# Performance work log

Hardware: AMD Instinct MI355X
Metric: run time of the kernel (lower is better)

Reference implementation:

```python
import jax, jax.numpy as jnp
import numpy as np

B, K, D, H, A = 8192, 10, 64, 128, 16
E = K * (K - 1)
# lexicographic ordered pairs (i,j), i != j -- matches adj.nonzero() and sorted(Dict.keys())
_PAIRS = np.array([(i, j) for i in range(K) for j in range(K) if i != j], dtype=np.int32)
SRC = jnp.asarray(_PAIRS[:, 0])  # message for edge (i,j) is aggregated at node i (row)
DST = jnp.asarray(_PAIRS[:, 1])


def setup_inputs() -> dict:
    key = jax.random.key(0)
    k1, k2, k3, k4, k5, k6 = jax.random.split(key, 6)
    F = D + H + A  # node MLP input dim
    return {
        "states": jax.random.normal(k1, (B, K, D), jnp.float32),
        "action_vec": jax.random.normal(k2, (B, K, A), jnp.float32),
        # one Linear(2D -> H) per ordered pair, stacked [E, 2D, H]
        "W_edge": jax.random.normal(k3, (E, 2 * D, H), jnp.float32) * (1.0 / np.sqrt(2 * D)),
        "b_edge": jax.random.normal(k4, (E, H), jnp.float32) * 0.01,
        # one Linear(D+H+A -> D) per node, stacked [K, F, D]
        "W_node": jax.random.normal(k5, (K, F, D), jnp.float32) * (1.0 / np.sqrt(F)),
        "b_node": jax.random.normal(k6, (K, D), jnp.float32) * 0.01,
    }


def reference(states, action_vec, W_edge, b_edge, W_node, b_node):
    # states: [B,K,D], action_vec: [B,K,A]
    b, k, d = states.shape
    # gather endpoints per ordered edge: [B,E,2D]
    pair_feat = jnp.concatenate([states[:, SRC, :], states[:, DST, :]], axis=-1)
    # per-edge-type Linear + tanh, batched as one grouped GEMM: [B,E,H]
    msg = jnp.tanh(jnp.einsum('bef,efh->beh', pair_feat, W_edge) + b_edge)
    # unsorted_segment_sum over source node index (row): [B,K,H]
    agg = jnp.zeros((b, k, msg.shape[-1]), msg.dtype).at[:, SRC, :].add(msg)
    # node input: [x, action, agg] -> per-node Linear + tanh: [B,K,D]
    node_in = jnp.concatenate([states, action_vec, agg], axis=-1)
    out = jnp.tanh(jnp.einsum('bkf,kfd->bkd', node_in, W_node) + b_node)
    return out
```

## Files before the change

kernel.cpp:

```cpp
#include <hip/hip_runtime.h>

typedef _Float16 f16;
typedef _Float16 f16x4 __attribute__((ext_vector_type(4)));
typedef _Float16 f16x8 __attribute__((ext_vector_type(8)));
typedef float    f32x4 __attribute__((ext_vector_type(4)));

#define S2C 2.88539008177792681472f

#define OFF_STF  0u
#define OFF_AC   5242880u
#define OFF_WEF  6553600u
#define OFF_WNF  8028160u
#define OFF_BE2  8171520u
#define OFF_Z    8195840u

__device__ __forceinline__ float fast_exp2(float x){
#if __has_builtin(__builtin_amdgcn_exp2f)
    return __builtin_amdgcn_exp2f(x);
#else
    return exp2f(x);
#endif
}
__device__ __forceinline__ float fast_rcp(float x){
#if __has_builtin(__builtin_amdgcn_rcpf)
    return __builtin_amdgcn_rcpf(x);
#else
    return 1.0f/x;
#endif
}

#define MFMA16(a,b,c) __builtin_amdgcn_mfma_f32_16x16x32_f16(a,b,c,0,0,0)

#define GLD16(g, l) __builtin_amdgcn_global_load_lds( \
    (const __attribute__((address_space(1))) void*)(g), \
    (__attribute__((address_space(3))) void*)(l), 16, 0, 0)

__global__ void prep(const float* __restrict__ st, const float* __restrict__ ac,
                     const float* __restrict__ We, const float* __restrict__ be,
                     const float* __restrict__ Wn, const float* __restrict__ bn,
                     f16* __restrict__ ws16){
    const int bid = blockIdx.x, t = threadIdx.x;
    if (bid < 2560){
        int g = bid*256 + t;
        int lane = g&63, ks = (g>>6)&1, rt = (g>>7)&1, rg2 = (g>>8)&255, node = g>>16;
        int row = rg2*32 + rt*16 + (lane&15);
        int k   = ks*32 + (lane>>4)*8;
        const float* src = st + ((size_t)row*10 + node)*64 + k;
        const float4 v0 = *(const float4*)src;
        const float4 v1 = *(const float4*)(src+4);
        f16x8 h; h[0]=(f16)v0.x; h[1]=(f16)v0.y; h[2]=(f16)v0.z; h[3]=(f16)v0.w;
                 h[4]=(f16)v1.x; h[5]=(f16)v1.y; h[6]=(f16)v1.z; h[7]=(f16)v1.w;
        *(f16x8*)(ws16 + OFF_STF + (size_t)g*8) = h;
    } else if (bid < 3840){
        int g = (bid-2560)*256 + t;
        const float4 v = ((const float4*)ac)[g];
        f16x4 h; h[0]=(f16)v.x; h[1]=(f16)v.y; h[2]=(f16)v.z; h[3]=(f16)v.w;
        *(f16x4*)(ws16 + OFF_AC + (size_t)g*4) = h;
    } else if (bid < 4560){
        int g = (bid-3840)*256 + t;
        int l = g & 15, q = (g>>4)&3, cg = (g>>6)&7, ks = (g>>9)&3, e = g>>11;
        const float* src = We + e*16384 + (ks*32 + q*8)*128 + cg*16 + l;
        f16x8 h;
        #pragma unroll
        for (int u=0;u<8;u++) h[u] = (f16)src[u*128];
        *(f16x8*)(ws16 + OFF_WEF + (size_t)g*8) = h;
    } else if (bid < 4630){
        int g = (bid-4560)*256 + t;
        if (g < 17920){
            int l = g&15, q=(g>>4)&3, c=(g>>6)&3, r=g>>8;
            int ks2 = r % 7, kn = r / 7;
            f16x8 h;
            #pragma unroll
            for (int u=0;u<8;u++){
                int knew = ks2*32 + q*8 + u;
                int f = (knew < 128) ? (knew + 80) : (knew - 128);
                h[u] = (knew < 208) ? (f16)Wn[kn*13312 + f*64 + c*16 + l] : (f16)0.0f;
            }
            *(f16x8*)(ws16 + OFF_WNF + (size_t)kn*14336 + ((size_t)(ks2*4+c)*64 + q*16 + l)*8) = h;
        }
    } else {
        int g = (bid-4630)*256 + t;
        float* be2 = (float*)(ws16 + OFF_BE2);
        if (g < 11520)      be2[g] = S2C*be[g];
        else if (g < 12160) be2[g] = S2C*bn[g-11520];
        else if (g < 12168) ws16[OFF_Z + (g-12160)] = (f16)0.0f;
    }
}

__launch_bounds__(512, 2)
__global__ void gnn_main(const f16* __restrict__ ws16, float* __restrict__ out){
    __shared__ alignas(16) f16 sW0[16384];
    __shared__ alignas(16) f16 sW1[16384];

    const f16* stf = ws16 + OFF_STF;
    const f16* Wef = ws16 + OFF_WEF;
    const float* be2 = (const float*)(ws16 + OFF_BE2);
    const float* bn2 = be2 + 11520;

    const int t = threadIdx.x, lane = t&63, wid = t>>6;
    const int l15 = lane&15, q = lane>>4, qo = q<<3;
    const int rg = wid>>1, cs = wid&1;

    const int swz = (blockIdx.x & 7)*80 + (blockIdx.x >> 3);
    const int rb  = swz / 10;
    const int i   = swz - rb*10;
    const int e0  = 9*i;
    const int rbrow = rb*4 + rg;

    {
        const f16* wsrc = Wef + (size_t)e0*16384 + (size_t)(wid*4)*512 + (size_t)lane*8;
        #pragma unroll
        for (int c=0; c<4; ++c)
            GLD16(wsrc + c*512, sW0 + (wid*4 + c)*512);
    }
    f16x8 ai[4];
    {
        const f16* p = stf + ((size_t)i*256 + rbrow)*2048 + lane*8;
        ai[0] = *(const f16x8*)p;        ai[1] = *(const f16x8*)(p+512);
        ai[2] = *(const f16x8*)(p+1024); ai[3] = *(const f16x8*)(p+1536);
    }
    __syncthreads();

    f32x4 agg[2][4] = {};

    #pragma unroll 1
    for (int e=0; e<9; ++e){
        const int ebase = e0 + e;
        f16* sWc = (e&1) ? sW1 : sW0;
        f16* sWn = (e&1) ? sW0 : sW1;

        const int j = e + (e >= i);
        const f16* pj = stf + ((size_t)j*256 + rbrow)*2048 + lane*8;
        f16x8 aj[4];
        aj[0] = *(const f16x8*)pj;        aj[1] = *(const f16x8*)(pj+512);
        aj[2] = *(const f16x8*)(pj+1024); aj[3] = *(const f16x8*)(pj+1536);
        float bv[4];
        #pragma unroll
        for (int c=0; c<4; ++c) bv[c] = be2[ebase*128 + cs*64 + c*16 + l15];

        if (e < 8){
            const f16* wsrc = Wef + (size_t)(ebase+1)*16384 + (size_t)(wid*4)*512 + (size_t)lane*8;
            #pragma unroll
            for (int c=0; c<4; ++c)
                GLD16(wsrc + c*512, sWn + (wid*4 + c)*512);
        } else {
            const f16* wnf = ws16 + OFF_WNF + (size_t)i*14336 + wid*512 + lane*8;
            #pragma unroll
            for (int c2=0; c2<4; ++c2){
                int m = c2*8 + wid;
                if (m < 28) GLD16(wnf + c2*4096, sWn + m*512);
            }
        }

        const f16* wb = sWc + cs*2048 + lane*8;
        #pragma unroll
        for (int rt=0; rt<2; ++rt){
            f32x4 msg[4] = {};
            #pragma unroll
            for (int ks4=0; ks4<4; ++ks4){
                f16x8 a = (ks4 < 2) ? ai[rt*2 + ks4] : aj[rt*2 + (ks4-2)];
                #pragma unroll
                for (int c=0; c<4; ++c){
                    f16x8 b = *(const f16x8*)(wb + (ks4*8 + c)*512);
                    msg[c] = MFMA16(a, b, msg[c]);
                }
            }
            #pragma unroll
            for (int c=0; c<4; ++c)
                #pragma unroll
                for (int r2=0; r2<4; ++r2){
                    float tt = __builtin_fmaf(msg[c][r2], S2C, bv[c]);
                    float rr = fast_rcp(fast_exp2(tt) + 1.0f);
                    agg[rt][c][r2] = __builtin_fmaf(-2.0f, rr, agg[rt][c][r2]);
                }
        }

        __syncthreads();
    }


    #pragma unroll
    for (int rt=0; rt<2; ++rt)
        #pragma unroll
        for (int c=0; c<4; ++c)
            #pragma unroll
            for (int r2=0; r2<4; ++r2){
                int lrow = rg*32 + rt*16 + q*4 + r2;
                int col  = cs*64 + c*16 + l15;
                sW0[lrow*128 + (((col>>3) ^ (lrow&7))<<3) + (col&7)] = (f16)(agg[rt][c][r2] + 9.0f);
            }
    __syncthreads();

    f32x4 acc[4] = {};
    const f16* acp = ws16 + OFF_AC;
    const f16* zb  = ws16 + OFF_Z;
    const int b0 = rb*128;
    #pragma unroll
    for (int ks2=0; ks2<7; ++ks2){
        f16x8 a;
        if (ks2 < 4){
            int lrow = wid*16 + l15;
            a = *(const f16x8*)(sW0 + lrow*128 + (((ks2*4 + q) ^ (l15&7))<<3));
        } else if (ks2 < 6){
            a = *(const f16x8*)(stf + ((size_t)i*256 + rb*4 + (wid>>1))*2048
                                + (wid&1)*1024 + (ks2-4)*512 + lane*8);
        } else {
            int row = b0 + wid*16 + l15;
            const f16* ap = (q < 2) ? (acp + ((size_t)row*10 + i)*16 + qo) : zb;
            a = *(const f16x8*)ap;
        }
        #pragma unroll
        for (int c=0; c<4; ++c){
            f16x8 bf = *(const f16x8*)(sW1 + (ks2*4+c)*512 + lane*8);
            acc[c] = MFMA16(a, bf, acc[c]);
        }
    }
    float bnv[4];
    #pragma unroll
    for (int c=0; c<4; ++c) bnv[c] = bn2[i*64 + c*16 + l15];
    #pragma unroll
    for (int c=0; c<4; ++c)
        #pragma unroll
        for (int r2=0; r2<4; ++r2){
            int row = b0 + wid*16 + q*4 + r2;
            int col = c*16 + l15;
            float tt = __builtin_fmaf(acc[c][r2], S2C, bnv[c]);
            float rr = fast_rcp(fast_exp2(tt) + 1.0f);
            out[((size_t)row*10 + i)*64 + col] = __builtin_fmaf(-2.0f, rr, 1.0f);
        }
}

extern "C" void kernel_launch(void* const* d_in, const int* in_sizes, int n_in,
                              void* d_out, int out_size, void* d_ws, size_t ws_size,
                              hipStream_t stream) {
    const float* states = (const float*)d_in[0];
    const float* action = (const float*)d_in[1];
    const float* W_edge = (const float*)d_in[2];
    const float* b_edge = (const float*)d_in[3];
    const float* W_node = (const float*)d_in[4];
    const float* b_node = (const float*)d_in[5];
    f16* ws16 = (f16*)d_ws;

    hipLaunchKernelGGL(prep, dim3(4678), dim3(256), 0, stream,
                       states, action, W_edge, b_edge, W_node, b_node, ws16);
    hipLaunchKernelGGL(gnn_main, dim3(640), dim3(512), 0, stream,
                       ws16, (float*)d_out);
}
```

Before: 144.3 us.

## Restructure edge loop to process two edges per stage with full-width waves

Each wave now owns 16 rows and all 128 hidden columns, instead of 32 rows split across two column halves. Edge weights are double-buffered two edges at a time in a 128KB shared buffer, and all ten node feature fragments are preloaded into registers, so the per-edge global loads of neighbour states go away. The tanh epilogue pairs two values to share one reciprocal, and the self-node fragment is reused from registers in the node MLP. In exchange, occupancy drops to one block per CU (launch bounds 512,1) and register pressure rises from the 20 preloaded fragments and 8 accumulators.

```diff
diff --git a/kernel.cpp b/kernel.cpp
--- a/kernel.cpp
+++ b/kernel.cpp
@@ -87,10 +87,41 @@
     }
 }
 
-__launch_bounds__(512, 2)
+__device__ __forceinline__ void edge_body(const f16* buf, int ebuf,
+        const float* __restrict__ be2, int eb, int l15, int lane,
+        const f16x8& a0, const f16x8& a1, const f16x8& a2, const f16x8& a3,
+        f32x4 (&agg)[8]){
+    float bv[8];
+    #pragma unroll
+    for (int c=0; c<8; ++c) bv[c] = be2[eb*128 + c*16 + l15];
+    const f16* wb = buf + ebuf*16384 + lane*8;
+    f32x4 msg[8] = {};
+    #pragma unroll
+    for (int c=0; c<8; ++c) msg[c] = MFMA16(a0, *(const f16x8*)(wb + ( 0 + c)*512), msg[c]);
+    #pragma unroll
+    for (int c=0; c<8; ++c) msg[c] = MFMA16(a1, *(const f16x8*)(wb + ( 8 + c)*512), msg[c]);
+    #pragma unroll
+    for (int c=0; c<8; ++c) msg[c] = MFMA16(a2, *(const f16x8*)(wb + (16 + c)*512), msg[c]);
+    #pragma unroll
+    for (int c=0; c<8; ++c) msg[c] = MFMA16(a3, *(const f16x8*)(wb + (24 + c)*512), msg[c]);
+    #pragma unroll
+    for (int c=0; c<8; ++c){
+        #pragma unroll
+        for (int r2=0; r2<4; r2+=2){
+            float t0 = __builtin_fminf(__builtin_fmaf(msg[c][r2],   S2C, bv[c]), 60.0f);
+            float t1 = __builtin_fminf(__builtin_fmaf(msg[c][r2+1], S2C, bv[c]), 60.0f);
+            float a0v = fast_exp2(t0) + 1.0f;
+            float a1v = fast_exp2(t1) + 1.0f;
+            float r   = fast_rcp(a0v*a1v);
+            agg[c][r2]   = __builtin_fmaf(-2.0f*a1v, r, agg[c][r2]);
+            agg[c][r2+1] = __builtin_fmaf(-2.0f*a0v, r, agg[c][r2+1]);
+        }
+    }
+}
+
+__launch_bounds__(512, 1)
 __global__ void gnn_main(const f16* __restrict__ ws16, float* __restrict__ out){
-    __shared__ alignas(16) f16 sW0[16384];
-    __shared__ alignas(16) f16 sW1[16384];
+    __shared__ alignas(16) f16 sW[65536];
 
     const f16* stf = ws16 + OFF_STF;
     const f16* Wef = ws16 + OFF_WEF;
@@ -99,80 +130,78 @@
 
     const int t = threadIdx.x, lane = t&63, wid = t>>6;
     const int l15 = lane&15, q = lane>>4, qo = q<<3;
-    const int rg = wid>>1, cs = wid&1;
 
     const int swz = (blockIdx.x & 7)*80 + (blockIdx.x >> 3);
     const int rb  = swz / 10;
     const int i   = swz - rb*10;
     const int e0  = 9*i;
-    const int rbrow = rb*4 + rg;
 
     {
-        const f16* wsrc = Wef + (size_t)e0*16384 + (size_t)(wid*4)*512 + (size_t)lane*8;
-        #pragma unroll
-        for (int c=0; c<4; ++c)
-            GLD16(wsrc + c*512, sW0 + (wid*4 + c)*512);
-    }
-    f16x8 ai[4];
-    {
-        const f16* p = stf + ((size_t)i*256 + rbrow)*2048 + lane*8;
-        ai[0] = *(const f16x8*)p;        ai[1] = *(const f16x8*)(p+512);
-        ai[2] = *(const f16x8*)(p+1024); ai[3] = *(const f16x8*)(p+1536);
-    }
+        #pragma unroll
+        for (int u=0; u<8; ++u){
+            int id = wid*8 + u;
+            int e  = id>>5, r = id&31;
+            GLD16(Wef + (size_t)(e0 + e)*16384 + r*512 + (size_t)lane*8,
+                  sW + e*16384 + r*512);
+        }
+    }
+    const f16* afb = stf + (size_t)(rb*4 + (wid>>1))*2048 + (wid&1)*1024 + (size_t)lane*8;
+    f16x8 aF[10][2];
+    #pragma unroll
+    for (int n=0; n<10; ++n){
+        aF[n][0] = *(const f16x8*)(afb + (size_t)n*524288);
+        aF[n][1] = *(const f16x8*)(afb + (size_t)n*524288 + 512);
+    }
+    f16x8 ai0, ai1;
+    #pragma unroll
+    for (int n=0; n<10; ++n)
+        if (n == i){ ai0 = aF[n][0]; ai1 = aF[n][1]; }
     __syncthreads();
 
-    f32x4 agg[2][4] = {};
+    f32x4 agg[8] = {};
 
     #pragma unroll 1
-    for (int e=0; e<9; ++e){
-        const int ebase = e0 + e;
-        f16* sWc = (e&1) ? sW1 : sW0;
-        f16* sWn = (e&1) ? sW0 : sW1;
-
-        const int j = e + (e >= i);
-        const f16* pj = stf + ((size_t)j*256 + rbrow)*2048 + lane*8;
-        f16x8 aj[4];
-        aj[0] = *(const f16x8*)pj;        aj[1] = *(const f16x8*)(pj+512);
-        aj[2] = *(const f16x8*)(pj+1024); aj[3] = *(const f16x8*)(pj+1536);
-        float bv[4];
-        #pragma unroll
-        for (int c=0; c<4; ++c) bv[c] = be2[ebase*128 + cs*64 + c*16 + l15];
-
-        if (e < 8){
-            const f16* wsrc = Wef + (size_t)(ebase+1)*16384 + (size_t)(wid*4)*512 + (size_t)lane*8;
-            #pragma unroll
-            for (int c=0; c<4; ++c)
-                GLD16(wsrc + c*512, sWn + (wid*4 + c)*512);
+    for (int p=0; p<5; ++p){
+        const f16* bufc = sW + (p&1)*32768;
+        f16*       bufn = sW + ((p+1)&1)*32768;
+
+        if (p < 4){
+            const int pe = (p+1)*2;
+            if (p < 3){
+                #pragma unroll
+                for (int u=0; u<8; ++u){
+                    int id = wid*8 + u;
+                    int e  = id>>5, r = id&31;
+                    GLD16(Wef + (size_t)(e0 + pe + e)*16384 + r*512 + (size_t)lane*8,
+                          bufn + e*16384 + r*512);
+                }
+            } else {
+                #pragma unroll
+                for (int u=0; u<4; ++u){
+                    int r = wid*4 + u;
+                    GLD16(Wef + (size_t)(e0 + 8)*16384 + r*512 + (size_t)lane*8,
+                          bufn + r*512);
+                }
+            }
         } else {
-            const f16* wnf = ws16 + OFF_WNF + (size_t)i*14336 + wid*512 + lane*8;
+            const f16* wnf = ws16 + OFF_WNF + (size_t)i*14336 + (size_t)lane*8;
             #pragma unroll
             for (int c2=0; c2<4; ++c2){
                 int m = c2*8 + wid;
-                if (m < 28) GLD16(wnf + c2*4096, sWn + m*512);
-            }
-        }
-
-        const f16* wb = sWc + cs*2048 + lane*8;
-        #pragma unroll
-        for (int rt=0; rt<2; ++rt){
-            f32x4 msg[4] = {};
-            #pragma unroll
-            for (int ks4=0; ks4<4; ++ks4){
-                f16x8 a = (ks4 < 2) ? ai[rt*2 + ks4] : aj[rt*2 + (ks4-2)];
-                #pragma unroll
-                for (int c=0; c<4; ++c){
-                    f16x8 b = *(const f16x8*)(wb + (ks4*8 + c)*512);
-                    msg[c] = MFMA16(a, b, msg[c]);
+                if (m < 28) GLD16(wnf + m*512, bufn + m*512);
+            }
+        }
+
+        #pragma unroll
+        for (int j=0; j<10; ++j){
+            const bool possible = ((j>>1) == p) || (j >= 1 && (((j-1)>>1) == p));
+            if (possible){
+                if (j != i && ((j - (j > i)) >> 1) == p){
+                    const int s = j - (j > i);
+                    edge_body(bufc, s&1, be2, e0 + s, l15, lane,
+                              ai0, ai1, aF[j][0], aF[j][1], agg);
                 }
             }
-            #pragma unroll
-            for (int c=0; c<4; ++c)
-                #pragma unroll
-                for (int r2=0; r2<4; ++r2){
-                    float tt = __builtin_fmaf(msg[c][r2], S2C, bv[c]);
-                    float rr = fast_rcp(fast_exp2(tt) + 1.0f);
-                    agg[rt][c][r2] = __builtin_fmaf(-2.0f, rr, agg[rt][c][r2]);
-                }
         }
 
         __syncthreads();
@@ -180,15 +209,13 @@
 
 
     #pragma unroll
-    for (int rt=0; rt<2; ++rt)
-        #pragma unroll
-        for (int c=0; c<4; ++c)
-            #pragma unroll
-            for (int r2=0; r2<4; ++r2){
-                int lrow = rg*32 + rt*16 + q*4 + r2;
-                int col  = cs*64 + c*16 + l15;
-                sW0[lrow*128 + (((col>>3) ^ (lrow&7))<<3) + (col&7)] = (f16)(agg[rt][c][r2] + 9.0f);
-            }
+    for (int ac=0; ac<8; ++ac)
+        #pragma unroll
+        for (int r2=0; r2<4; ++r2){
+            int lrow = wid*16 + q*4 + r2;
+            int col  = ac*16 + l15;
+            sW[lrow*128 + (((col>>3) ^ (lrow&7))<<3) + (col&7)] = (f16)(agg[ac][r2] + 9.0f);
+        }
     __syncthreads();
 
     f32x4 acc[4] = {};
@@ -200,10 +227,11 @@
         f16x8 a;
         if (ks2 < 4){
             int lrow = wid*16 + l15;
-            a = *(const f16x8*)(sW0 + lrow*128 + (((ks2*4 + q) ^ (l15&7))<<3));
-        } else if (ks2 < 6){
-            a = *(const f16x8*)(stf + ((size_t)i*256 + rb*4 + (wid>>1))*2048
-                                + (wid&1)*1024 + (ks2-4)*512 + lane*8);
+            a = *(const f16x8*)(sW + lrow*128 + (((ks2*4 + q) ^ (l15&7))<<3));
+        } else if (ks2 == 4){
+            a = ai0;
+        } else if (ks2 == 5){
+            a = ai1;
         } else {
             int row = b0 + wid*16 + l15;
             const f16* ap = (q < 2) ? (acp + ((size_t)row*10 + i)*16 + qo) : zb;
@@ -211,7 +239,7 @@
         }
         #pragma unroll
         for (int c=0; c<4; ++c){
-            f16x8 bf = *(const f16x8*)(sW1 + (ks2*4+c)*512 + lane*8);
+            f16x8 bf = *(const f16x8*)(sW + 32768 + (ks2*4+c)*512 + lane*8);
             acc[c] = MFMA16(a, bf, acc[c]);
         }
     }
```

Result: slower. 161.6 us (+12.0%).
